# Kernel optimization log

Measured on AMD Instinct MI355X. Metric: run time of the kernel, lower is better.

## Reference

```python
import jax, jax.numpy as jnp
import numpy as np

T, B, N, D = 32, 8, 256, 512
TAU = 2.0   # LIF membrane time constant
VTH = 1.0   # spike threshold
ALPHA = 4.0 # surrogate-gradient sharpness


def setup_inputs() -> dict:
    key = jax.random.key(0)
    k0, k1, k2 = jax.random.split(key, 3)
    scale = 1.0 / np.sqrt(D)
    return {
        "x": jax.random.normal(k0, (T, B, N, D), jnp.float32),
        "tr_mx": jnp.zeros((B, N, D), jnp.float32),            # initial membrane state
        "W_lif": jax.random.normal(k1, (D, D), jnp.float32) * scale,
        "b_lif": jnp.zeros((D,), jnp.float32),
        "W_rec": jax.random.normal(k2, (D, D), jnp.float32) * scale,  # recon2 weight (d_ff=D -> patch_size=D)
        "b_rec": jnp.zeros((D,), jnp.float32),
    }


def _spike(v):
    # Heaviside forward, sigmoid surrogate backward (standard SNN straight-through)
    s = jax.nn.sigmoid(ALPHA * v)
    return s + jax.lax.stop_gradient((v > 0).astype(v.dtype) - s)


def reference(x, tr_mx, W_lif, b_lif, W_rec, b_rec):
    # MemoryUpdate.replay: tau-decayed LIF recurrence over time, emitting spike gate per step
    inp = jnp.einsum('tbnd,de->tbne', x, W_lif) + b_lif   # [T,B,N,D] input current

    def step(mem, i_t):
        mem = mem + (i_t - mem) / TAU        # leaky integration
        sp = _spike(mem - VTH)               # fire
        mem = mem * (1.0 - sp)               # hard reset
        return mem, sp

    _, sp_seq = jax.lax.scan(step, tr_mx, inp)  # sp_seq: [T,B,N,D]

    g = x * (1.0 - sp_seq)                       # gated residual
    rec_x = jnp.einsum('tbnd,dp->tbnp', g, W_rec) + b_rec  # recon2 on flattened (T*B, N, D)
    return rec_x
```

## Files before the change

kernel.cpp:

```cpp
#include <hip/hip_runtime.h>
#include <hip/hip_bf16.h>


#define TT 32
#define CH 8
#define BB 8
#define NN 256
#define DD 512

typedef __attribute__((ext_vector_type(8))) short short8;
typedef __attribute__((ext_vector_type(4))) float f32x4;

__device__ __forceinline__ unsigned short f2bf(float f) {
    __hip_bfloat16 h = __float2bfloat16(f);
    return *reinterpret_cast<unsigned short*>(&h);
}

__global__ void cast_transpose_wr(const float* __restrict__ Wr,
                                  unsigned short* __restrict__ Wt) {
    int idx = blockIdx.x * 256 + threadIdx.x;
    int d = idx >> 9;
    int p = idx & 511;
    Wt[p * DD + d] = f2bf(Wr[idx]);
}

__global__ __launch_bounds__(128, 4) void lif_phaseA_g(
    const float* __restrict__ x,
    const float* __restrict__ tr_mx,
    const float* __restrict__ Wl,
    const float* __restrict__ bl,
    unsigned short* __restrict__ gws)
{
    __shared__ __align__(16) float xs[CH * DD];

    const int tid = threadIdx.x;
    const int tok = blockIdx.x;
    const int e0  = tid * 4;
    const size_t base = (size_t)tok * DD;
    const size_t st   = (size_t)BB * NN * DD;

    float acc[CH][4];
    float4 m4 = *reinterpret_cast<const float4*>(&tr_mx[base + e0]);
    float m[4] = {m4.x, m4.y, m4.z, m4.w};

    const float4 blv = *reinterpret_cast<const float4*>(&bl[e0]);
    const float blr[4] = {blv.x, blv.y, blv.z, blv.w};

    #pragma unroll 1
    for (int tg = 0; tg < 4; ++tg) {
        #pragma unroll
        for (int r = 0; r < 8; ++r) {
            const int flat = r * 128 + tid;
            const int row  = flat >> 7;
            const int c4   = flat & 127;
            const float4 v = *reinterpret_cast<const float4*>(
                &x[(size_t)(tg * CH + row) * st + base + c4 * 4]);
            *reinterpret_cast<float4*>(&xs[row * DD + c4 * 4]) = v;
        }
        __syncthreads();

        #pragma unroll
        for (int i = 0; i < CH; ++i)
            #pragma unroll
            for (int e = 0; e < 4; ++e) acc[i][e] = blr[e];

        #pragma unroll 2
        for (int d = 0; d < DD; d += 4) {
            const float4 w0 = *reinterpret_cast<const float4*>(&Wl[(size_t)(d + 0) * DD + e0]);
            const float4 w1 = *reinterpret_cast<const float4*>(&Wl[(size_t)(d + 1) * DD + e0]);
            const float4 w2 = *reinterpret_cast<const float4*>(&Wl[(size_t)(d + 2) * DD + e0]);
            const float4 w3 = *reinterpret_cast<const float4*>(&Wl[(size_t)(d + 3) * DD + e0]);
            #pragma unroll
            for (int i = 0; i < CH; ++i) {
                const float4 xv = *reinterpret_cast<const float4*>(&xs[i * DD + d]);
                acc[i][0] = fmaf(xv.x, w0.x, acc[i][0]);
                acc[i][1] = fmaf(xv.x, w0.y, acc[i][1]);
                acc[i][2] = fmaf(xv.x, w0.z, acc[i][2]);
                acc[i][3] = fmaf(xv.x, w0.w, acc[i][3]);
                acc[i][0] = fmaf(xv.y, w1.x, acc[i][0]);
                acc[i][1] = fmaf(xv.y, w1.y, acc[i][1]);
                acc[i][2] = fmaf(xv.y, w1.z, acc[i][2]);
                acc[i][3] = fmaf(xv.y, w1.w, acc[i][3]);
                acc[i][0] = fmaf(xv.z, w2.x, acc[i][0]);
                acc[i][1] = fmaf(xv.z, w2.y, acc[i][1]);
                acc[i][2] = fmaf(xv.z, w2.z, acc[i][2]);
                acc[i][3] = fmaf(xv.z, w2.w, acc[i][3]);
                acc[i][0] = fmaf(xv.w, w3.x, acc[i][0]);
                acc[i][1] = fmaf(xv.w, w3.y, acc[i][1]);
                acc[i][2] = fmaf(xv.w, w3.z, acc[i][2]);
                acc[i][3] = fmaf(xv.w, w3.w, acc[i][3]);
            }
        }
        __syncthreads();

        #pragma unroll
        for (int i = 0; i < CH; ++i) {
            const int t = tg * CH + i;
            const float4 xv = *reinterpret_cast<const float4*>(&xs[i * DD + e0]);
            float g[4];
            const float xr[4] = {xv.x, xv.y, xv.z, xv.w};
            #pragma unroll
            for (int e = 0; e < 4; ++e) {
                m[e] = m[e] + (acc[i][e] - m[e]) * 0.5f;
                const float s = (m[e] - 1.0f > 0.0f) ? 1.0f : 0.0f;
                g[e] = (s > 0.0f) ? 0.0f : xr[e];
                m[e] *= (1.0f - s);
            }
            uint2 p;
            p.x = (unsigned)f2bf(g[0]) | ((unsigned)f2bf(g[1]) << 16);
            p.y = (unsigned)f2bf(g[2]) | ((unsigned)f2bf(g[3]) << 16);
            *reinterpret_cast<uint2*>(&gws[((size_t)tok * TT + t) * DD + e0]) = p;
        }
        __syncthreads();
    }
}

__global__ __launch_bounds__(512, 2) void lif_phaseB3(
    const unsigned short* __restrict__ gws,
    const unsigned short* __restrict__ Wt,
    const float* __restrict__ br,
    float* __restrict__ out)
{
    const int tid = threadIdx.x;
    const int tok = blockIdx.x;
    const int w    = tid >> 6;
    const int lane = tid & 63;
    const int hB   = w & 1;
    const int q    = w >> 1;
    const int lcol = lane & 15;
    const int lkg  = lane >> 4;
    const int tA   = hB * 16 + lcol;
    const size_t st = (size_t)BB * NN * DD;
    const int colb = q * 128;

    const unsigned short* arow = &gws[((size_t)tok * TT + tA) * DD];

    f32x4 acc[8];
    #pragma unroll
    for (int nt = 0; nt < 8; ++nt) {
        const float b = br[colb + nt * 16 + lcol];
        acc[nt] = (f32x4){b, b, b, b};
    }

    #pragma unroll 1
    for (int ks = 0; ks < 16; ++ks) {
        const int kb = ks * 32 + lkg * 8;
        const short8 a = *reinterpret_cast<const short8*>(&arow[kb]);
        #pragma unroll
        for (int nt = 0; nt < 8; ++nt) {
            const int col = colb + nt * 16 + lcol;
            const short8 bf = *reinterpret_cast<const short8*>(&Wt[(size_t)col * DD + kb]);
            acc[nt] = __builtin_amdgcn_mfma_f32_16x16x32_bf16(a, bf, acc[nt], 0, 0, 0);
        }
    }

    #pragma unroll
    for (int nt = 0; nt < 8; ++nt) {
        const int col = colb + nt * 16 + lcol;
        #pragma unroll
        for (int r = 0; r < 4; ++r) {
            const int t = hB * 16 + lkg * 4 + r;
            out[(size_t)t * st + (size_t)tok * DD + col] = acc[nt][r];
        }
    }
}

__global__ __launch_bounds__(128, 4) void lif_phaseA_m(
    const float* __restrict__ x, const float* __restrict__ tr_mx,
    const float* __restrict__ Wl, const float* __restrict__ bl,
    unsigned* __restrict__ gmsk)
{
    __shared__ __align__(16) float xs[CH * 256];

    const int tid = threadIdx.x;
    const int tok = blockIdx.x;
    const int e0  = tid * 4;
    const size_t base = (size_t)tok * DD;
    const size_t st   = (size_t)BB * NN * DD;

    float acc[CH][4];
    float4 m4 = *reinterpret_cast<const float4*>(&tr_mx[base + e0]);
    float m[4] = {m4.x, m4.y, m4.z, m4.w};
    unsigned mc[4] = {0u, 0u, 0u, 0u};
    const float4 blv = *reinterpret_cast<const float4*>(&bl[e0]);
    const float blr[4] = {blv.x, blv.y, blv.z, blv.w};

    #pragma unroll 1
    for (int tg = 0; tg < 4; ++tg) {
        #pragma unroll
        for (int i = 0; i < CH; ++i)
            #pragma unroll
            for (int e = 0; e < 4; ++e) acc[i][e] = blr[e];

        #pragma unroll 1
        for (int h = 0; h < 2; ++h) {
            #pragma unroll
            for (int r = 0; r < 4; ++r) {
                const int flat = r * 128 + tid;
                const int row  = flat >> 6;
                const int c4   = flat & 63;
                const float4 v = *reinterpret_cast<const float4*>(
                    &x[(size_t)(tg * CH + row) * st + base + h * 256 + c4 * 4]);
                *reinterpret_cast<float4*>(&xs[row * 256 + c4 * 4]) = v;
            }
            __syncthreads();

            #pragma unroll 2
            for (int dd_ = 0; dd_ < 256; dd_ += 4) {
                const int d = h * 256 + dd_;
                const float4 w0 = *reinterpret_cast<const float4*>(&Wl[(size_t)(d + 0) * DD + e0]);
                const float4 w1 = *reinterpret_cast<const float4*>(&Wl[(size_t)(d + 1) * DD + e0]);
                const float4 w2 = *reinterpret_cast<const float4*>(&Wl[(size_t)(d + 2) * DD + e0]);
                const float4 w3 = *reinterpret_cast<const float4*>(&Wl[(size_t)(d + 3) * DD + e0]);
                #pragma unroll
                for (int i = 0; i < CH; ++i) {
                    const float4 xv = *reinterpret_cast<const float4*>(&xs[i * 256 + dd_]);
                    acc[i][0] = fmaf(xv.x, w0.x, acc[i][0]);
                    acc[i][1] = fmaf(xv.x, w0.y, acc[i][1]);
                    acc[i][2] = fmaf(xv.x, w0.z, acc[i][2]);
                    acc[i][3] = fmaf(xv.x, w0.w, acc[i][3]);
                    acc[i][0] = fmaf(xv.y, w1.x, acc[i][0]);
                    acc[i][1] = fmaf(xv.y, w1.y, acc[i][1]);
                    acc[i][2] = fmaf(xv.y, w1.z, acc[i][2]);
                    acc[i][3] = fmaf(xv.y, w1.w, acc[i][3]);
                    acc[i][0] = fmaf(xv.z, w2.x, acc[i][0]);
                    acc[i][1] = fmaf(xv.z, w2.y, acc[i][1]);
                    acc[i][2] = fmaf(xv.z, w2.z, acc[i][2]);
                    acc[i][3] = fmaf(xv.z, w2.w, acc[i][3]);
                    acc[i][0] = fmaf(xv.w, w3.x, acc[i][0]);
                    acc[i][1] = fmaf(xv.w, w3.y, acc[i][1]);
                    acc[i][2] = fmaf(xv.w, w3.z, acc[i][2]);
                    acc[i][3] = fmaf(xv.w, w3.w, acc[i][3]);
                }
            }
            __syncthreads();
        }

        #pragma unroll
        for (int i = 0; i < CH; ++i) {
            const int t = tg * CH + i;
            #pragma unroll
            for (int e = 0; e < 4; ++e) {
                m[e] = m[e] + (acc[i][e] - m[e]) * 0.5f;
                const float s = (m[e] - 1.0f > 0.0f) ? 1.0f : 0.0f;
                mc[e] |= (s > 0.0f) ? (1u << t) : 0u;
                m[e] *= (1.0f - s);
            }
        }
    }

    uint4 mv;
    mv.x = mc[0]; mv.y = mc[1]; mv.z = mc[2]; mv.w = mc[3];
    *reinterpret_cast<uint4*>(&gmsk[base + e0]) = mv;
}

template<bool UW>
__global__ __launch_bounds__(256, 2) void lif_phaseB2(
    const float* __restrict__ x, const float* __restrict__ Wr,
    const float* __restrict__ br, const unsigned short* __restrict__ Wt,
    const unsigned* __restrict__ gmsk, float* __restrict__ out)
{
    __shared__ __align__(16) unsigned ms[2 * DD];

    const int tid = threadIdx.x;
    const size_t st = (size_t)BB * NN * DD;
    {
        const uint4 v = *reinterpret_cast<const uint4*>(
            &gmsk[(size_t)blockIdx.x * 2 * DD + tid * 4]);
        *reinterpret_cast<uint4*>(&ms[tid * 4]) = v;
    }
    __syncthreads();

    const int wv   = tid >> 6;
    const int lane = tid & 63;
    const int qB   = wv >> 1;
    const int hB   = wv & 1;
    const int lcol = lane & 15;
    const int lkg  = lane >> 4;
    const int tA   = hB * 16 + lcol;
    const size_t baseB = (size_t)(blockIdx.x * 2 + qB) * DD;
    const unsigned* mq = &ms[qB * DD];
    const float* xrow = &x[(size_t)tA * st + baseB];

    #pragma unroll 1
    for (int pass = 0; pass < 4; ++pass) {
        const int colb = pass * 128;
        f32x4 acc[8];
        #pragma unroll
        for (int nt = 0; nt < 8; ++nt) {
            const float b = br[colb + nt * 16 + lcol];
            acc[nt] = (f32x4){b, b, b, b};
        }
        #pragma unroll 1
        for (int ks = 0; ks < 16; ++ks) {
            const int kb = ks * 32 + lkg * 8;
            const float4 x0 = *reinterpret_cast<const float4*>(&xrow[kb]);
            const float4 x1 = *reinterpret_cast<const float4*>(&xrow[kb + 4]);
            const uint4 m0 = *reinterpret_cast<const uint4*>(&mq[kb]);
            const uint4 m1 = *reinterpret_cast<const uint4*>(&mq[kb + 4]);
            short8 a;
            a[0] = (short)f2bf(((m0.x >> tA) & 1u) ? 0.0f : x0.x);
            a[1] = (short)f2bf(((m0.y >> tA) & 1u) ? 0.0f : x0.y);
            a[2] = (short)f2bf(((m0.z >> tA) & 1u) ? 0.0f : x0.z);
            a[3] = (short)f2bf(((m0.w >> tA) & 1u) ? 0.0f : x0.w);
            a[4] = (short)f2bf(((m1.x >> tA) & 1u) ? 0.0f : x1.x);
            a[5] = (short)f2bf(((m1.y >> tA) & 1u) ? 0.0f : x1.y);
            a[6] = (short)f2bf(((m1.z >> tA) & 1u) ? 0.0f : x1.z);
            a[7] = (short)f2bf(((m1.w >> tA) & 1u) ? 0.0f : x1.w);
            #pragma unroll
            for (int nt = 0; nt < 8; ++nt) {
                const int col = colb + nt * 16 + lcol;
                short8 bf;
                if (UW) {
                    bf = *reinterpret_cast<const short8*>(&Wt[(size_t)col * DD + kb]);
                } else {
                    #pragma unroll
                    for (int j = 0; j < 8; ++j)
                        bf[j] = (short)f2bf(Wr[(size_t)(kb + j) * DD + col]);
                }
                acc[nt] = __builtin_amdgcn_mfma_f32_16x16x32_bf16(a, bf, acc[nt], 0, 0, 0);
            }
        }
        #pragma unroll
        for (int nt = 0; nt < 8; ++nt) {
            const int col = colb + nt * 16 + lcol;
            #pragma unroll
            for (int r = 0; r < 4; ++r) {
                const int t = hB * 16 + lkg * 4 + r;
                out[(size_t)t * st + baseB + col] = acc[nt][r];
            }
        }
    }
}

extern "C" void kernel_launch(void* const* d_in, const int* in_sizes, int n_in,
                              void* d_out, int out_size, void* d_ws, size_t ws_size,
                              hipStream_t stream) {
    const float* x     = (const float*)d_in[0];
    const float* tr_mx = (const float*)d_in[1];
    const float* Wl    = (const float*)d_in[2];
    const float* bl    = (const float*)d_in[3];
    const float* Wr    = (const float*)d_in[4];
    const float* br    = (const float*)d_in[5];
    float* out = (float*)d_out;

    const size_t g_bytes   = (size_t)BB * NN * TT * DD * 2;
    const size_t wt_bytes  = (size_t)DD * DD * 2;
    const size_t msk_bytes = (size_t)BB * NN * DD * 4;

    if (ws_size >= g_bytes + wt_bytes) {
        unsigned short* gws = (unsigned short*)d_ws;
        unsigned short* Wt  = (unsigned short*)((char*)d_ws + g_bytes);
        cast_transpose_wr<<<dim3(1024), dim3(256), 0, stream>>>(Wr, Wt);
        lif_phaseA_g<<<dim3(BB * NN), dim3(128), 0, stream>>>(x, tr_mx, Wl, bl, gws);
        lif_phaseB3<<<dim3(BB * NN), dim3(512), 0, stream>>>(gws, Wt, br, out);
    } else if (ws_size >= msk_bytes + wt_bytes) {
        unsigned* gmsk = (unsigned*)d_ws;
        unsigned short* Wt = (unsigned short*)((char*)d_ws + msk_bytes);
        cast_transpose_wr<<<dim3(1024), dim3(256), 0, stream>>>(Wr, Wt);
        lif_phaseA_m<<<dim3(BB * NN), dim3(128), 0, stream>>>(x, tr_mx, Wl, bl, gmsk);
        lif_phaseB2<true><<<dim3(BB * NN / 2), dim3(256), 0, stream>>>(x, Wr, br, Wt, gmsk, out);
    } else if (ws_size >= msk_bytes) {
        unsigned* gmsk = (unsigned*)d_ws;
        lif_phaseA_m<<<dim3(BB * NN), dim3(128), 0, stream>>>(x, tr_mx, Wl, bl, gmsk);
        lif_phaseB2<false><<<dim3(BB * NN / 2), dim3(256), 0, stream>>>(x, Wr, br, nullptr, gmsk, out);
    }
}
```

Before: 763.8 us.

## Process four tokens per block in phase A and two tokens per block in phase B

Phase A now runs 512-thread blocks that each handle four tokens. The four tokens' 128-thread groups share L1/L2 reuse of the W_lif rows, and a block-wide barrier after the FMA loop is removed because each group reads only its own shared-memory slice. Phase B computes two tokens per block, so each loaded W_rec bf16 fragment feeds two MFMAs. This halves weight-fragment loads per output, at the cost of doubling the accumulator registers and the LDS footprint (64KB per block in phase A), which may reduce occupancy.

```diff
diff --git a/kernel.cpp b/kernel.cpp
--- a/kernel.cpp
+++ b/kernel.cpp
@@ -24,18 +24,20 @@
     Wt[p * DD + d] = f2bf(Wr[idx]);
 }
 
-__global__ __launch_bounds__(128, 4) void lif_phaseA_g(
+__global__ __launch_bounds__(512, 4) void lif_phaseA_g4(
     const float* __restrict__ x,
     const float* __restrict__ tr_mx,
     const float* __restrict__ Wl,
     const float* __restrict__ bl,
     unsigned short* __restrict__ gws)
 {
-    __shared__ __align__(16) float xs[CH * DD];
+    __shared__ __align__(16) float xs[4 * CH * DD];
 
     const int tid = threadIdx.x;
-    const int tok = blockIdx.x;
-    const int e0  = tid * 4;
+    const int tq  = tid >> 7;
+    const int tl  = tid & 127;
+    const int e0  = tl * 4;
+    const int tok = blockIdx.x * 4 + tq;
     const size_t base = (size_t)tok * DD;
     const size_t st   = (size_t)BB * NN * DD;
 
@@ -50,12 +52,15 @@
     for (int tg = 0; tg < 4; ++tg) {
         #pragma unroll
         for (int r = 0; r < 8; ++r) {
-            const int flat = r * 128 + tid;
-            const int row  = flat >> 7;
-            const int c4   = flat & 127;
+            const int flat = r * 512 + tid;
+            const int q    = flat >> 10;
+            const int rem  = flat & 1023;
+            const int row  = rem >> 7;
+            const int c4   = rem & 127;
             const float4 v = *reinterpret_cast<const float4*>(
-                &x[(size_t)(tg * CH + row) * st + base + c4 * 4]);
-            *reinterpret_cast<float4*>(&xs[row * DD + c4 * 4]) = v;
+                &x[(size_t)(tg * CH + row) * st
+                   + (size_t)(blockIdx.x * 4 + q) * DD + c4 * 4]);
+            *reinterpret_cast<float4*>(&xs[(q * CH + row) * DD + c4 * 4]) = v;
         }
         __syncthreads();
 
@@ -63,6 +68,8 @@
         for (int i = 0; i < CH; ++i)
             #pragma unroll
             for (int e = 0; e < 4; ++e) acc[i][e] = blr[e];
+
+        const float* xsl = &xs[tq * CH * DD];
 
         #pragma unroll 2
         for (int d = 0; d < DD; d += 4) {
@@ -72,7 +79,7 @@
             const float4 w3 = *reinterpret_cast<const float4*>(&Wl[(size_t)(d + 3) * DD + e0]);
             #pragma unroll
             for (int i = 0; i < CH; ++i) {
-                const float4 xv = *reinterpret_cast<const float4*>(&xs[i * DD + d]);
+                const float4 xv = *reinterpret_cast<const float4*>(&xsl[i * DD + d]);
                 acc[i][0] = fmaf(xv.x, w0.x, acc[i][0]);
                 acc[i][1] = fmaf(xv.x, w0.y, acc[i][1]);
                 acc[i][2] = fmaf(xv.x, w0.z, acc[i][2]);
@@ -91,12 +98,11 @@
                 acc[i][3] = fmaf(xv.w, w3.w, acc[i][3]);
             }
         }
-        __syncthreads();
 
         #pragma unroll
         for (int i = 0; i < CH; ++i) {
             const int t = tg * CH + i;
-            const float4 xv = *reinterpret_cast<const float4*>(&xs[i * DD + e0]);
+            const float4 xv = *reinterpret_cast<const float4*>(&xsl[i * DD + e0]);
             float g[4];
             const float xr[4] = {xv.x, xv.y, xv.z, xv.w};
             #pragma unroll
@@ -115,14 +121,13 @@
     }
 }
 
-__global__ __launch_bounds__(512, 2) void lif_phaseB3(
+__global__ __launch_bounds__(512, 2) void lif_phaseB4(
     const unsigned short* __restrict__ gws,
     const unsigned short* __restrict__ Wt,
     const float* __restrict__ br,
     float* __restrict__ out)
 {
     const int tid = threadIdx.x;
-    const int tok = blockIdx.x;
     const int w    = tid >> 6;
     const int lane = tid & 63;
     const int hB   = w & 1;
@@ -132,25 +137,30 @@
     const int tA   = hB * 16 + lcol;
     const size_t st = (size_t)BB * NN * DD;
     const int colb = q * 128;
-
-    const unsigned short* arow = &gws[((size_t)tok * TT + tA) * DD];
-
-    f32x4 acc[8];
+    const int tok0 = blockIdx.x * 2;
+
+    const unsigned short* arow0 = &gws[((size_t)tok0 * TT + tA) * DD];
+    const unsigned short* arow1 = &gws[((size_t)(tok0 + 1) * TT + tA) * DD];
+
+    f32x4 acc0[8], acc1[8];
     #pragma unroll
     for (int nt = 0; nt < 8; ++nt) {
         const float b = br[colb + nt * 16 + lcol];
-        acc[nt] = (f32x4){b, b, b, b};
+        acc0[nt] = (f32x4){b, b, b, b};
+        acc1[nt] = (f32x4){b, b, b, b};
     }
 
     #pragma unroll 1
     for (int ks = 0; ks < 16; ++ks) {
         const int kb = ks * 32 + lkg * 8;
-        const short8 a = *reinterpret_cast<const short8*>(&arow[kb]);
+        const short8 a0 = *reinterpret_cast<const short8*>(&arow0[kb]);
+        const short8 a1 = *reinterpret_cast<const short8*>(&arow1[kb]);
         #pragma unroll
         for (int nt = 0; nt < 8; ++nt) {
             const int col = colb + nt * 16 + lcol;
             const short8 bf = *reinterpret_cast<const short8*>(&Wt[(size_t)col * DD + kb]);
-            acc[nt] = __builtin_amdgcn_mfma_f32_16x16x32_bf16(a, bf, acc[nt], 0, 0, 0);
+            acc0[nt] = __builtin_amdgcn_mfma_f32_16x16x32_bf16(a0, bf, acc0[nt], 0, 0, 0);
+            acc1[nt] = __builtin_amdgcn_mfma_f32_16x16x32_bf16(a1, bf, acc1[nt], 0, 0, 0);
         }
     }
 
@@ -160,7 +170,8 @@
         #pragma unroll
         for (int r = 0; r < 4; ++r) {
             const int t = hB * 16 + lkg * 4 + r;
-            out[(size_t)t * st + (size_t)tok * DD + col] = acc[nt][r];
+            out[(size_t)t * st + (size_t)tok0 * DD + col]       = acc0[nt][r];
+            out[(size_t)t * st + (size_t)(tok0 + 1) * DD + col] = acc1[nt][r];
         }
     }
 }
@@ -352,8 +363,8 @@
         unsigned short* gws = (unsigned short*)d_ws;
         unsigned short* Wt  = (unsigned short*)((char*)d_ws + g_bytes);
         cast_transpose_wr<<<dim3(1024), dim3(256), 0, stream>>>(Wr, Wt);
-        lif_phaseA_g<<<dim3(BB * NN), dim3(128), 0, stream>>>(x, tr_mx, Wl, bl, gws);
-        lif_phaseB3<<<dim3(BB * NN), dim3(512), 0, stream>>>(gws, Wt, br, out);
+        lif_phaseA_g4<<<dim3(BB * NN / 4), dim3(512), 0, stream>>>(x, tr_mx, Wl, bl, gws);
+        lif_phaseB4<<<dim3(BB * NN / 2), dim3(512), 0, stream>>>(gws, Wt, br, out);
     } else if (ws_size >= msk_bytes + wt_bytes) {
         unsigned* gmsk = (unsigned*)d_ws;
         unsigned short* Wt = (unsigned short*)((char*)d_ws + msk_bytes);
```

Result: faster. 625.8 us (median of 3 runs) (-18.1%).
